# Kernel optimization log

Measured on AMD Instinct MI355X. Metric: run time of the kernel, lower is better.

## Reference

```python
import jax, jax.numpy as jnp
import numpy as np

NH = 8        # num_heads
KS = 64       # key_size
C_IN = 256
C_OUT = 3 * NH * KS   # 1536
GROUPS = 3 * NH       # 24
EPS = 1e-5
H = W = 64


def setup_inputs() -> dict:
    key = jax.random.key(0)
    k1, k2 = jax.random.split(key)
    x = jax.random.normal(k1, (1, C_IN, H, W), dtype=jnp.float32)
    conv_w = jax.random.normal(k2, (C_OUT, C_IN, 1, 1), dtype=jnp.float32) * 0.05
    gn_w = jnp.ones((C_OUT,), dtype=jnp.float32)
    gn_b = jnp.zeros((C_OUT,), dtype=jnp.float32)
    return {"x": x, "conv_w": conv_w, "gn_w": gn_w, "gn_b": gn_b}


def reference(x, conv_w, gn_w, gn_b):
    B, _, h, w = x.shape
    # 1x1 conv (normalize=True -> no bias): per-pixel GEMM over channels
    attn = jnp.einsum('bchw,oc->bohw', x, conv_w[:, :, 0, 0])  # [B, 1536, H, W]
    # GroupNorm: 24 groups of KS channels, normalized over (KS, H, W)
    g = attn.reshape(B, GROUPS, -1)
    mean = g.mean(axis=-1, keepdims=True)
    var = g.var(axis=-1, keepdims=True)
    g = (g - mean) * jax.lax.rsqrt(var + EPS)
    attn = g.reshape(B, C_OUT, h, w) * gn_w[None, :, None, None] + gn_b[None, :, None, None]
    # split into key, query, value (in that order, per chunk(3, dim=2))
    attn = attn.reshape(B, NH, 3 * KS, h * w)
    key_, query, value = jnp.split(attn, 3, axis=2)   # each [B, NH, KS, HW]
    # saliency = q^T @ k / sqrt(KS) -> [B, NH, HW, HW]
    saliency = jnp.einsum('bnkq,bnkl->bnql', query, key_) / jnp.sqrt(jnp.float32(KS))
    mask = jax.nn.softmax(saliency, axis=-1)
    # out = v @ mask^T -> [B, NH, KS, HW]
    out = jnp.einsum('bnkl,bnql->bnkq', value, mask)
    return out.reshape(B, NH * KS, h, w)
```

## Files before the change

kernel.cpp:

```cpp
#include <hip/hip_runtime.h>

typedef __bf16 bf16;
typedef __bf16 bf16x8 __attribute__((ext_vector_type(8)));
typedef __bf16 bf16x4 __attribute__((ext_vector_type(4)));
typedef float f32x4 __attribute__((ext_vector_type(4)));
typedef float f32x16 __attribute__((ext_vector_type(16)));


#define QF 0.18033688011112042f
#define EXPF(x) __builtin_amdgcn_exp2f(x)

union U4 { bf16x4 v; unsigned u[2]; };
union U8 { bf16x8 v; unsigned u[4]; };

__global__ void k_misc(const float* __restrict__ x, const float* __restrict__ w,
                       bf16* __restrict__ xT, bf16* __restrict__ wb, float* __restrict__ cs) {
    int b = blockIdx.x;
    if (b < 512) {
        int t = b * 256 + threadIdx.x;
        int p  = t & 4095;
        int c0 = (t >> 12) * 8;
        bf16x8 o;
#pragma unroll
        for (int j = 0; j < 8; j++) o[j] = (bf16)x[(c0 + j) * 4096 + p];
        *(bf16x8*)(xT + p * 256 + c0) = o;
    } else if (b < 896) {
        int idx = ((b - 512) * 256 + threadIdx.x) * 4;
        float4 f = *(const float4*)(w + idx);
        bf16x4 o;
        o[0] = (bf16)f.x; o[1] = (bf16)f.y; o[2] = (bf16)f.z; o[3] = (bf16)f.w;
        *(bf16x4*)(wb + idx) = o;
    } else {
#pragma unroll
        for (int i = 0; i < 12; i++) cs[i * 256 + threadIdx.x] = 0.f;
    }
}

__global__ __launch_bounds__(256) void k_conv(const bf16* __restrict__ Wb,
                                              const bf16* __restrict__ xT,
                                              bf16* __restrict__ qkvT,
                                              float* __restrict__ cs) {
    __shared__ __attribute__((aligned(16))) bf16 xs[64 * 72];
    __shared__ __attribute__((aligned(16))) bf16 ws2[64 * 72];
    int wid = threadIdx.x >> 6, lane = threadIdx.x & 63;
    int quad = lane >> 4, l15 = lane & 15;
    int g  = blockIdx.x % 24;
    int pb = (blockIdx.x / 24) * 64;
    int h = g / 3, sec = g % 3;
    int ob = g * 64;

    int srow = threadIdx.x >> 2;
    int scol = (threadIdx.x & 3) * 16;

    f32x4 acc[4];
#pragma unroll
    for (int c = 0; c < 4; c++) acc[c] = (f32x4){0.f, 0.f, 0.f, 0.f};

    bf16x8 fx0 = *(const bf16x8*)(xT + (pb + srow) * 256 + scol);
    bf16x8 fx1 = *(const bf16x8*)(xT + (pb + srow) * 256 + scol + 8);
    bf16x8 fw0 = *(const bf16x8*)(Wb + (ob + srow) * 256 + scol);
    bf16x8 fw1 = *(const bf16x8*)(Wb + (ob + srow) * 256 + scol + 8);

    for (int c4 = 0; c4 < 4; c4++) {
        __syncthreads();
        *(bf16x8*)(xs  + srow * 72 + scol)     = fx0;
        *(bf16x8*)(xs  + srow * 72 + scol + 8) = fx1;
        *(bf16x8*)(ws2 + srow * 72 + scol)     = fw0;
        *(bf16x8*)(ws2 + srow * 72 + scol + 8) = fw1;
        __syncthreads();

        if (c4 < 3) {
            int co = (c4 + 1) * 64;
            fx0 = *(const bf16x8*)(xT + (pb + srow) * 256 + co + scol);
            fx1 = *(const bf16x8*)(xT + (pb + srow) * 256 + co + scol + 8);
            fw0 = *(const bf16x8*)(Wb + (ob + srow) * 256 + co + scol);
            fw1 = *(const bf16x8*)(Wb + (ob + srow) * 256 + co + scol + 8);
        }

#pragma unroll
        for (int k2 = 0; k2 < 2; k2++) {
            bf16x8 a = *(const bf16x8*)(ws2 + (wid * 16 + l15) * 72 + k2 * 32 + quad * 8);
#pragma unroll
            for (int c = 0; c < 4; c++) {
                bf16x8 b = *(const bf16x8*)(xs + (c * 16 + l15) * 72 + k2 * 32 + quad * 8);
                acc[c] = __builtin_amdgcn_mfma_f32_16x16x32_bf16(a, b, acc[c], 0, 0, 0);
            }
        }
    }

    int ch0 = wid * 16 + quad * 4;
#pragma unroll
    for (int r = 0; r < 4; r++) {
        float sp  = acc[0][r] + acc[1][r] + acc[2][r] + acc[3][r];
        float ssp = acc[0][r] * acc[0][r] + acc[1][r] * acc[1][r]
                  + acc[2][r] * acc[2][r] + acc[3][r] * acc[3][r];
#pragma unroll
        for (int m = 1; m < 16; m <<= 1) {
            sp  += __shfl_xor(sp,  m, 64);
            ssp += __shfl_xor(ssp, m, 64);
        }
        if (l15 == 0) {
            atomicAdd(cs + (ob + ch0 + r) * 2,     sp);
            atomicAdd(cs + (ob + ch0 + r) * 2 + 1, ssp);
        }
    }

    __syncthreads();
    bf16* tile = xs;
    if (sec == 2) {
#pragma unroll
        for (int c = 0; c < 4; c++)
#pragma unroll
            for (int r = 0; r < 4; r++)
                tile[(ch0 + r) * 72 + c * 16 + l15] = (bf16)acc[c][r];
    } else {
#pragma unroll
        for (int c = 0; c < 4; c++) {
            bf16x4 o;
#pragma unroll
            for (int r = 0; r < 4; r++) o[r] = (bf16)acc[c][r];
            *(bf16x4*)(&tile[(c * 16 + l15) * 72 + ch0]) = o;
        }
    }
    __syncthreads();
    bf16* base = qkvT + h * 786432;
    int t = threadIdx.x;
    if (sec == 2) {
        bf16* V = base + 524288;
#pragma unroll
        for (int it = 0; it < 2; it++) {
            int e = it * 256 + t; int ch = e >> 3; int pxo = (e & 7) * 8;
            *(bf16x8*)(V + ch * 4096 + pb + pxo) = *(const bf16x8*)(&tile[ch * 72 + pxo]);
        }
    } else {
        bf16* dst = base + (sec == 0 ? 262144 : 0);
#pragma unroll
        for (int it = 0; it < 2; it++) {
            int e = it * 256 + t; int px = e >> 3; int cho = (e & 7) * 8;
            *(bf16x8*)(dst + (pb + px) * 64 + cho) = *(const bf16x8*)(&tile[px * 72 + cho]);
        }
    }
}

#define PF_BLOCK(S, PFA, PFB)                                                   \
    {                                                                           \
        float p0 = EXPF(S[0]),  p1 = EXPF(S[1]),  p2 = EXPF(S[2]),  p3 = EXPF(S[3]);   \
        float p4 = EXPF(S[4]),  p5 = EXPF(S[5]),  p6 = EXPF(S[6]),  p7 = EXPF(S[7]);   \
        float p8 = EXPF(S[8]),  p9 = EXPF(S[9]),  p10 = EXPF(S[10]), p11 = EXPF(S[11]); \
        float p12 = EXPF(S[12]), p13 = EXPF(S[13]), p14 = EXPF(S[14]), p15 = EXPF(S[15]); \
        lacc += (((p0 + p1) + (p2 + p3)) + ((p4 + p5) + (p6 + p7)))             \
              + (((p8 + p9) + (p10 + p11)) + ((p12 + p13) + (p14 + p15)));      \
        U4 lo, hi;                                                              \
        lo.v[0] = (bf16)p0;  lo.v[1] = (bf16)p1;  lo.v[2] = (bf16)p2;  lo.v[3] = (bf16)p3;  \
        hi.v[0] = (bf16)p4;  hi.v[1] = (bf16)p5;  hi.v[2] = (bf16)p6;  hi.v[3] = (bf16)p7;  \
        unsigned a0 = lo.u[0], b0 = hi.u[0], a1 = lo.u[1], b1 = hi.u[1];        \
        asm("v_permlane32_swap_b32 %0, %1" : "+v"(a0), "+v"(b0));               \
        asm("v_permlane32_swap_b32 %0, %1" : "+v"(a1), "+v"(b1));               \
        U8 fA; fA.u[0] = a0; fA.u[1] = a1; fA.u[2] = b0; fA.u[3] = b1;          \
        PFA = fA.v;                                                             \
        U4 lo2, hi2;                                                            \
        lo2.v[0] = (bf16)p8;  lo2.v[1] = (bf16)p9;  lo2.v[2] = (bf16)p10; lo2.v[3] = (bf16)p11; \
        hi2.v[0] = (bf16)p12; hi2.v[1] = (bf16)p13; hi2.v[2] = (bf16)p14; hi2.v[3] = (bf16)p15; \
        unsigned a2 = lo2.u[0], b2 = hi2.u[0], a3 = lo2.u[1], b3 = hi2.u[1];    \
        asm("v_permlane32_swap_b32 %0, %1" : "+v"(a2), "+v"(b2));               \
        asm("v_permlane32_swap_b32 %0, %1" : "+v"(a3), "+v"(b3));               \
        U8 fB; fB.u[0] = a2; fB.u[1] = a3; fB.u[2] = b2; fB.u[3] = b3;          \
        PFB = fB.v;                                                             \
    }

__global__ __launch_bounds__(256, 4) void k_attn(const bf16* __restrict__ qkvT,
                                                 const float2* __restrict__ cs,
                                                 const float* __restrict__ gnw,
                                                 const float* __restrict__ gnb,
                                                 bf16* __restrict__ Opart,
                                                 float* __restrict__ Lsum) {
    int bid   = blockIdx.x;
    int h     = bid & 7;
    int qb    = (bid >> 3) & 31;
    int split = bid >> 8;
    int wid = threadIdx.x >> 6, lane = threadIdx.x & 63;
    int l31 = lane & 31, half = lane >> 5;
    const bf16* QT = qkvT + h * 786432;
    const bf16* KT = QT + 262144;
    const bf16* V  = QT + 524288;
    int qw = qb * 128 + wid * 32;

    __shared__ __attribute__((aligned(16))) bf16 Ks[2][64 * 72];
    __shared__ __attribute__((aligned(16))) bf16 Vs[2][64 * 72];

    int r0   = threadIdx.x >> 3;
    int koff = (threadIdx.x & 7) * 8;

    float2 vK = cs[(h * 3) * 64 + lane];
    float2 vQ = cs[(h * 3 + 1) * 64 + lane];
    float sK = vK.x, qK = vK.y, sQ = vQ.x, qQ = vQ.y;
#pragma unroll
    for (int m = 1; m < 64; m <<= 1) {
        sK += __shfl_xor(sK, m, 64); qK += __shfl_xor(qK, m, 64);
        sQ += __shfl_xor(sQ, m, 64); qQ += __shfl_xor(qQ, m, 64);
    }
    const float N = 262144.0f;
    float meanK = sK / N, invK = rsqrtf(qK / N - meanK * meanK + 1e-5f);
    float meanQ = sQ / N, invQ = rsqrtf(qQ / N - meanQ * meanQ + 1e-5f);

    float aK[8], bK[8];
#pragma unroll
    for (int j = 0; j < 8; j++) {
        float gw = gnw[h * 192 + koff + j] * invK;
        aK[j] = gw;
        bK[j] = gnb[h * 192 + koff + j] - meanK * gw;
    }

    bf16x8 bq[4];
#pragma unroll
    for (int ks = 0; ks < 4; ks++) {
        bf16x8 raw = *(const bf16x8*)(QT + (qw + l31) * 64 + ks * 16 + half * 8);
#pragma unroll
        for (int j = 0; j < 8; j++) {
            int c = ks * 16 + half * 8 + j;
            float gw = gnw[h * 192 + 64 + c] * invQ;
            float av = gw * QF;
            float bv = (gnb[h * 192 + 64 + c] - meanQ * gw) * QF;
            bq[ks][j] = (bf16)(av * (float)raw[j] + bv);
        }
    }

    f32x16 oacc0 = (f32x16)(0.0f), oacc1 = (f32x16)(0.0f);
    float ls = 0.f;

    int t0 = split * 16, t1 = t0 + 16;

    bf16x8 kf0, kf1, vf0, vf1;
    {
        int lb0 = t0 * 64;
        kf0 = *(const bf16x8*)(KT + (lb0 + r0) * 64 + koff);
        kf1 = *(const bf16x8*)(KT + (lb0 + r0 + 32) * 64 + koff);
        vf0 = *(const bf16x8*)(V + r0 * 4096 + lb0 + koff);
        vf1 = *(const bf16x8*)(V + (r0 + 32) * 4096 + lb0 + koff);
    }

    for (int lt = t0; lt < t1; lt++) {
        bf16* ksb = Ks[lt & 1];
        bf16* vsb = Vs[lt & 1];

        bf16x8 nk0, nk1;
#pragma unroll
        for (int j = 0; j < 8; j++) nk0[j] = (bf16)(aK[j] * (float)kf0[j] + bK[j]);
#pragma unroll
        for (int j = 0; j < 8; j++) nk1[j] = (bf16)(aK[j] * (float)kf1[j] + bK[j]);
        *(bf16x8*)(ksb + r0 * 72 + koff)        = nk0;
        *(bf16x8*)(ksb + (r0 + 32) * 72 + koff) = nk1;
        *(bf16x8*)(vsb + r0 * 72 + koff)        = vf0;
        *(bf16x8*)(vsb + (r0 + 32) * 72 + koff) = vf1;
        __syncthreads();

        if (lt + 1 < t1) {
            int nb = (lt + 1) * 64;
            kf0 = *(const bf16x8*)(KT + (nb + r0) * 64 + koff);
            kf1 = *(const bf16x8*)(KT + (nb + r0 + 32) * 64 + koff);
            vf0 = *(const bf16x8*)(V + r0 * 4096 + nb + koff);
            vf1 = *(const bf16x8*)(V + (r0 + 32) * 4096 + nb + koff);
        }

        const bf16* ka = ksb + l31 * 72 + half * 8;
        const bf16* kb = ksb + (32 + l31) * 72 + half * 8;
        f32x16 s0 = (f32x16)(0.0f), s1 = (f32x16)(0.0f);
        __builtin_amdgcn_s_setprio(1);
#pragma unroll
        for (int ks = 0; ks < 4; ks++) {
            s0 = __builtin_amdgcn_mfma_f32_32x32x16_bf16(
                *(const bf16x8*)(ka + ks * 16), bq[ks], s0, 0, 0, 0);
            s1 = __builtin_amdgcn_mfma_f32_32x32x16_bf16(
                *(const bf16x8*)(kb + ks * 16), bq[ks], s1, 0, 0, 0);
        }
        __builtin_amdgcn_s_setprio(0);

        float lacc = ls;
        bf16x8 pf0, pf1, pf2, pf3;
        PF_BLOCK(s0, pf0, pf1);
        PF_BLOCK(s1, pf2, pf3);
        ls = lacc;

        const bf16* va = vsb + l31 * 72 + half * 8;
        const bf16* vb = vsb + (32 + l31) * 72 + half * 8;
        __builtin_amdgcn_s_setprio(1);
        oacc0 = __builtin_amdgcn_mfma_f32_32x32x16_bf16(*(const bf16x8*)(va +  0), pf0, oacc0, 0, 0, 0);
        oacc1 = __builtin_amdgcn_mfma_f32_32x32x16_bf16(*(const bf16x8*)(vb +  0), pf0, oacc1, 0, 0, 0);
        oacc0 = __builtin_amdgcn_mfma_f32_32x32x16_bf16(*(const bf16x8*)(va + 16), pf1, oacc0, 0, 0, 0);
        oacc1 = __builtin_amdgcn_mfma_f32_32x32x16_bf16(*(const bf16x8*)(vb + 16), pf1, oacc1, 0, 0, 0);
        oacc0 = __builtin_amdgcn_mfma_f32_32x32x16_bf16(*(const bf16x8*)(va + 32), pf2, oacc0, 0, 0, 0);
        oacc1 = __builtin_amdgcn_mfma_f32_32x32x16_bf16(*(const bf16x8*)(vb + 32), pf2, oacc1, 0, 0, 0);
        oacc0 = __builtin_amdgcn_mfma_f32_32x32x16_bf16(*(const bf16x8*)(va + 48), pf3, oacc0, 0, 0, 0);
        oacc1 = __builtin_amdgcn_mfma_f32_32x32x16_bf16(*(const bf16x8*)(vb + 48), pf3, oacc1, 0, 0, 0);
        __builtin_amdgcn_s_setprio(0);
    }

    ls += __shfl_xor(ls, 32, 64);
    if (half == 0)
        Lsum[split * 32768 + h * 4096 + qw + l31] = ls;

    bf16* Ob = Opart + split * 2097152;
#pragma unroll
    for (int r = 0; r < 16; r++) {
        int kd = (r & 3) + 8 * (r >> 2) + 4 * half;
        Ob[(h * 64 + kd) * 4096 + qw + l31]        = (bf16)oacc0[r];
        Ob[(h * 64 + 32 + kd) * 4096 + qw + l31]   = (bf16)oacc1[r];
    }
}

__global__ void k_final(const bf16* __restrict__ Opart, const float* __restrict__ Lsum,
                        const float2* __restrict__ cs, const float* __restrict__ gnw,
                        const float* __restrict__ gnb, float* __restrict__ out) {
    int gid = blockIdx.x * 256 + threadIdx.x;
    int row = gid >> 9;
    int c8  = (gid & 511) << 3;
    int h   = row >> 6;

    int g = h * 3 + 2;
    int c = threadIdx.x & 63;
    float2 v = cs[g * 64 + c];
    float s = v.x, ss = v.y;
#pragma unroll
    for (int m = 1; m < 64; m <<= 1) { s += __shfl_xor(s, m, 64); ss += __shfl_xor(ss, m, 64); }
    const float N = 262144.0f;
    float mean = s / N;
    float inv  = rsqrtf(ss / N - mean * mean + 1e-5f);
    int gi = h * 192 + 128 + (row & 63);
    float gw = gnw[gi];
    float va = inv * gw;
    float vb = gnb[gi] - mean * inv * gw;

    float o[8] = {0, 0, 0, 0, 0, 0, 0, 0};
    float l[8] = {0, 0, 0, 0, 0, 0, 0, 0};
#pragma unroll
    for (int sp = 0; sp < 4; sp++) {
        bf16x8 vv = *(const bf16x8*)(Opart + sp * 2097152 + row * 4096 + c8);
        const float* L = Lsum + sp * 32768 + h * 4096 + c8;
        float4 l0 = *(const float4*)L;
        float4 l1 = *(const float4*)(L + 4);
#pragma unroll
        for (int j = 0; j < 8; j++) o[j] += (float)vv[j];
        l[0] += l0.x; l[1] += l0.y; l[2] += l0.z; l[3] += l0.w;
        l[4] += l1.x; l[5] += l1.y; l[6] += l1.z; l[7] += l1.w;
    }
    float4 r0, r1;
    r0.x = va * o[0] / l[0] + vb; r0.y = va * o[1] / l[1] + vb;
    r0.z = va * o[2] / l[2] + vb; r0.w = va * o[3] / l[3] + vb;
    r1.x = va * o[4] / l[4] + vb; r1.y = va * o[5] / l[5] + vb;
    r1.z = va * o[6] / l[6] + vb; r1.w = va * o[7] / l[7] + vb;
    *(float4*)(out + row * 4096 + c8)     = r0;
    *(float4*)(out + row * 4096 + c8 + 4) = r1;
}

extern "C" void kernel_launch(void* const* d_in, const int* in_sizes, int n_in,
                              void* d_out, int out_size, void* d_ws, size_t ws_size,
                              hipStream_t stream) {
    const float* x      = (const float*)d_in[0];
    const float* conv_w = (const float*)d_in[1];
    const float* gn_w   = (const float*)d_in[2];
    const float* gn_b   = (const float*)d_in[3];
    float* out = (float*)d_out;
    char* ws = (char*)d_ws;

    bf16*   qkvT  = (bf16*) (ws);
    bf16*   Opart = (bf16*) (ws + 12582912);
    bf16*   Wb    = (bf16*) (ws + 12582912);
    bf16*   xT    = (bf16*) (ws + 13369344);
    float*  Lsum  = (float*)(ws + 29360128);
    float*  cs    = (float*)(ws + 29884416);

    hipLaunchKernelGGL(k_misc,  dim3(897),  dim3(256), 0, stream, x, conv_w, xT, Wb, cs);
    hipLaunchKernelGGL(k_conv,  dim3(1536), dim3(256), 0, stream, Wb, xT, qkvT, cs);
    hipLaunchKernelGGL(k_attn,  dim3(1024), dim3(256), 0, stream, qkvT, (const float2*)cs,
                       gn_w, gn_b, Opart, Lsum);
    hipLaunchKernelGGL(k_final, dim3(1024), dim3(256), 0, stream, Opart, Lsum, (const float2*)cs, gn_w, gn_b, out);
}
```

Before: 144.5 us.

## Fold key GroupNorm scale into query and tile the input transpose through LDS

The per-channel key GroupNorm affine is removed from the inner attention loop. The key scale is folded into the normalized query, and the key shift is dropped because it only adds a per-query constant to the scores, which softmax cancels. The input transpose in k_misc now goes through a 64x64 shared-memory tile, so both global reads and writes are coalesced, and the grid shrinks accordingly. The shift drop holds only because softmax is shift-invariant per row. Raw bf16 keys with the scale applied to q may change rounding slightly.

```diff
diff --git a/kernel.cpp b/kernel.cpp
--- a/kernel.cpp
+++ b/kernel.cpp
@@ -16,16 +16,31 @@
 __global__ void k_misc(const float* __restrict__ x, const float* __restrict__ w,
                        bf16* __restrict__ xT, bf16* __restrict__ wb, float* __restrict__ cs) {
     int b = blockIdx.x;
-    if (b < 512) {
-        int t = b * 256 + threadIdx.x;
-        int p  = t & 4095;
-        int c0 = (t >> 12) * 8;
-        bf16x8 o;
-#pragma unroll
-        for (int j = 0; j < 8; j++) o[j] = (bf16)x[(c0 + j) * 4096 + p];
-        *(bf16x8*)(xT + p * 256 + c0) = o;
-    } else if (b < 896) {
-        int idx = ((b - 512) * 256 + threadIdx.x) * 4;
+    if (b < 256) {
+        __shared__ float ld[64][65];
+        int cb = (b & 3) * 64;
+        int pb = (b >> 2) * 64;
+        int tp = (threadIdx.x & 15) * 4;
+        int tc = threadIdx.x >> 4;
+#pragma unroll
+        for (int pass = 0; pass < 4; pass++) {
+            int c = tc + pass * 16;
+            float4 f = *(const float4*)(x + (cb + c) * 4096 + pb + tp);
+            ld[tp][c] = f.x; ld[tp + 1][c] = f.y; ld[tp + 2][c] = f.z; ld[tp + 3][c] = f.w;
+        }
+        __syncthreads();
+        int px = threadIdx.x >> 3;
+        int co = (threadIdx.x & 7) * 8;
+#pragma unroll
+        for (int pass = 0; pass < 2; pass++) {
+            int p2 = px + pass * 32;
+            bf16x8 o;
+#pragma unroll
+            for (int j = 0; j < 8; j++) o[j] = (bf16)ld[p2][co + j];
+            *(bf16x8*)(xT + (pb + p2) * 256 + cb + co) = o;
+        }
+    } else if (b < 640) {
+        int idx = ((b - 256) * 256 + threadIdx.x) * 4;
         float4 f = *(const float4*)(w + idx);
         bf16x4 o;
         o[0] = (bf16)f.x; o[1] = (bf16)f.y; o[2] = (bf16)f.z; o[3] = (bf16)f.w;
@@ -203,14 +218,6 @@
     float meanK = sK / N, invK = rsqrtf(qK / N - meanK * meanK + 1e-5f);
     float meanQ = sQ / N, invQ = rsqrtf(qQ / N - meanQ * meanQ + 1e-5f);
 
-    float aK[8], bK[8];
-#pragma unroll
-    for (int j = 0; j < 8; j++) {
-        float gw = gnw[h * 192 + koff + j] * invK;
-        aK[j] = gw;
-        bK[j] = gnb[h * 192 + koff + j] - meanK * gw;
-    }
-
     bf16x8 bq[4];
 #pragma unroll
     for (int ks = 0; ks < 4; ks++) {
@@ -218,10 +225,10 @@
 #pragma unroll
         for (int j = 0; j < 8; j++) {
             int c = ks * 16 + half * 8 + j;
-            float gw = gnw[h * 192 + 64 + c] * invQ;
-            float av = gw * QF;
-            float bv = (gnb[h * 192 + 64 + c] - meanQ * gw) * QF;
-            bq[ks][j] = (bf16)(av * (float)raw[j] + bv);
+            float gwq = gnw[h * 192 + 64 + c] * invQ;
+            float qv  = (gwq * (float)raw[j] + (gnb[h * 192 + 64 + c] - meanQ * gwq)) * QF;
+            float aKc = gnw[h * 192 + c] * invK;
+            bq[ks][j] = (bf16)(aKc * qv);
         }
     }
 
@@ -243,13 +250,8 @@
         bf16* ksb = Ks[lt & 1];
         bf16* vsb = Vs[lt & 1];
 
-        bf16x8 nk0, nk1;
-#pragma unroll
-        for (int j = 0; j < 8; j++) nk0[j] = (bf16)(aK[j] * (float)kf0[j] + bK[j]);
-#pragma unroll
-        for (int j = 0; j < 8; j++) nk1[j] = (bf16)(aK[j] * (float)kf1[j] + bK[j]);
-        *(bf16x8*)(ksb + r0 * 72 + koff)        = nk0;
-        *(bf16x8*)(ksb + (r0 + 32) * 72 + koff) = nk1;
+        *(bf16x8*)(ksb + r0 * 72 + koff)        = kf0;
+        *(bf16x8*)(ksb + (r0 + 32) * 72 + koff) = kf1;
         *(bf16x8*)(vsb + r0 * 72 + koff)        = vf0;
         *(bf16x8*)(vsb + (r0 + 32) * 72 + koff) = vf1;
         __syncthreads();
@@ -369,7 +371,7 @@
     float*  Lsum  = (float*)(ws + 29360128);
     float*  cs    = (float*)(ws + 29884416);
 
-    hipLaunchKernelGGL(k_misc,  dim3(897),  dim3(256), 0, stream, x, conv_w, xT, Wb, cs);
+    hipLaunchKernelGGL(k_misc,  dim3(641),  dim3(256), 0, stream, x, conv_w, xT, Wb, cs);
     hipLaunchKernelGGL(k_conv,  dim3(1536), dim3(256), 0, stream, Wb, xT, qkvT, cs);
     hipLaunchKernelGGL(k_attn,  dim3(1024), dim3(256), 0, stream, qkvT, (const float2*)cs,
                        gn_w, gn_b, Opart, Lsum);
```

Result: faster. 133.5 us (-7.6%).
